# Optimization experiments

Measured on AMD Instinct MI355X. Metric: run time of the kernel, lower is better.

The kernel has to match this reference:

```python
import jax, jax.numpy as jnp
import numpy as np

H_PARAM = 3.0   # filtering strength h
TWS = 5         # template window size
SWS = 11        # search window size


def _shift_stack(x, window_size):
    # [N,C,H,W] -> [N,C,H,W,window_size**2] of circularly shifted copies.
    # Shift order matches the torch module: outer loop x_shift, inner y_shift,
    # roll shifts=(y_shift, x_shift) on dims (H, W).
    r = window_size // 2
    return jnp.stack(
        [jnp.roll(x, (ys, xs), axis=(2, 3))
         for xs in range(-r, r + 1) for ys in range(-r, r + 1)],
        axis=-1,
    )


def _box_filter(x, window_size):
    # Circular box-sum over H,W dims. The torch double roll loop is separable,
    # so do it as two 1-D roll sums (10 rolls instead of 25 for tws=5).
    r = window_size // 2
    s = x
    acc = x
    for k in range(1, r + 1):
        acc = acc + jnp.roll(s, k, axis=3) + jnp.roll(s, -k, axis=3)
    s2 = acc
    for k in range(1, r + 1):
        acc = acc + jnp.roll(s2, k, axis=2) + jnp.roll(s2, -k, axis=2)
    return acc


def setup_inputs() -> dict:
    key = jax.random.key(0)
    x = jax.random.uniform(key, (2, 3, 512, 512), dtype=jnp.float32)
    return {"x": x}


def reference(x):
    # luminance (RGB input: C == 3)
    xc = jnp.clip(x, 0.0, 1.0)
    y = 0.299 * xc[:, :1] + 0.587 * xc[:, 1:2] + 0.114 * xc[:, 2:3]  # [N,1,H,W]

    x_stack = _shift_stack(x, SWS)  # [N,3,H,W,sws^2]
    y_stack = _shift_stack(y, SWS)  # [N,1,H,W,sws^2]

    d2 = _box_filter((y[..., None] - y_stack) ** 2, TWS)  # [N,1,H,W,sws^2]
    distances = jnp.sqrt(d2)
    weights = jnp.exp(-distances / H_PARAM)                # [N,1,H,W,sws^2]

    denoised = (weights * x_stack).sum(axis=-1) / weights.sum(axis=-1)
    return jnp.clip(denoised, 0.0, 1.0)
```

## Files before the change

kernel.cpp:

```cpp
#include <hip/hip_runtime.h>
#include <math.h>


#define H_IMG 512
#define W_IMG 512
#define MASK  511
#define HWSZ  (H_IMG * W_IMG)
#define TILE  32
#define HALO  7
#define XD    46
#define YSTR  48
#define HSTR  44

__global__ __launch_bounds__(256, 2)
void nlm_kernel(const float* __restrict__ x, float* __restrict__ out) {
    __shared__ float4 ldsX[XD * XD];
    __shared__ float  ldsY[XD * YSTR];
    __shared__ float  ldsH[XD * HSTR];

    const int n  = blockIdx.z;
    const int ti = blockIdx.y * TILE;
    const int tj = blockIdx.x * TILE;
    const int tx = threadIdx.x;
    const int ty = threadIdx.y;
    const int tid = ty * 32 + tx;

    const float* xb = x + (size_t)n * 3 * HWSZ;

    for (int e = tid; e < XD * XD; e += 256) {
        int r = e / XD, c = e - r * XD;
        int gi = (ti + r - HALO) & MASK;
        int gj = (tj + c - HALO) & MASK;
        size_t o = (size_t)gi * W_IMG + gj;
        ldsX[e] = make_float4(xb[o], xb[o + HWSZ], xb[o + 2 * HWSZ], 0.f);
    }
    __syncthreads();

    for (int e = tid; e < XD * XD; e += 256) {
        float4 v = ldsX[e];
        float r = fminf(fmaxf(v.x, 0.f), 1.f);
        float g = fminf(fmaxf(v.y, 0.f), 1.f);
        float b = fminf(fmaxf(v.z, 0.f), 1.f);
        int rr = e / XD, cc = e - rr * XD;
        ldsY[rr * YSTR + cc] = 0.299f * r + 0.587f * g + 0.114f * b;
    }
    __syncthreads();

    for (int e = tid; e < XD * 42; e += 256) {
        int r = e / 42, c = e - r * 42;
        const float* yr = &ldsY[r * YSTR + c];
        float a0 = yr[0], a1 = yr[1], a2 = yr[2], a3 = yr[3], a4 = yr[4];
        ldsH[r * HSTR + c] = a0*a0 + a1*a1 + a2*a2 + a3*a3 + a4*a4;
    }
    __syncthreads();

    const int jl = tx + HALO;
    const int il = ty * 4 + HALO;

    float cy[8][5];
    float hc[8];
    #pragma unroll
    for (int t = 0; t < 8; ++t) {
        #pragma unroll
        for (int c = 0; c < 5; ++c)
            cy[t][c] = ldsY[(il - 2 + t) * YSTR + (jl - 2 + c)];
        hc[t] = ldsH[(il - 2 + t) * HSTR + (jl - 2)];
    }

    float den[4]  = {0.f, 0.f, 0.f, 0.f};
    float num0[4] = {0.f, 0.f, 0.f, 0.f};
    float num1[4] = {0.f, 0.f, 0.f, 0.f};
    float num2[4] = {0.f, 0.f, 0.f, 0.f};

    #pragma unroll 1
    for (int xs = -5; xs <= 5; ++xs) {
        const int jc  = jl - xs - 2;
        const int xjc = jl - xs;

        float  sw[8][5];
        float  Hs[8];
        float4 xw[4];

        #pragma unroll
        for (int t = 0; t < 8; ++t) {
            #pragma unroll
            for (int c = 0; c < 5; ++c)
                sw[t][c] = ldsY[(il - 7 + t) * YSTR + jc + c];
            Hs[t] = ldsH[(il - 7 + t) * HSTR + jc];
        }
        #pragma unroll
        for (int t = 0; t < 4; ++t)
            xw[t] = ldsX[(il - 5 + t) * XD + xjc];

        #pragma unroll
        for (int k = 0; k <= 10; ++k) {
            float nsw[5], nHs;
            float4 nxw;
            if (k < 10) {
                const int nr = il + k + 1;
                #pragma unroll
                for (int c = 0; c < 5; ++c) nsw[c] = ldsY[nr * YSTR + jc + c];
                nHs = ldsH[nr * HSTR + jc];
                nxw = ldsX[(il + k - 1) * XD + xjc];
            }

            float h[8];
            #pragma unroll
            for (int t = 0; t < 8; ++t) {
                const int m = (t + k) & 7;
                float s = 0.f;
                #pragma unroll
                for (int c = 0; c < 5; ++c)
                    s = fmaf(cy[t][c], sw[m][c], s);
                h[t] = fmaf(-2.f, s, hc[t] + Hs[m]);
            }

            float d2 = h[0] + h[1] + h[2] + h[3] + h[4];
            #pragma unroll
            for (int o = 0; o < 4; ++o) {
                if (o > 0) d2 += h[o + 4] - h[o - 1];
                float d2c = fmaxf(d2, 0.f);
                float w = __expf(__builtin_amdgcn_sqrtf(d2c) * (-1.0f / 3.0f));
                float4 xv = xw[(k + o) & 3];
                num0[o] = fmaf(w, xv.x, num0[o]);
                num1[o] = fmaf(w, xv.y, num1[o]);
                num2[o] = fmaf(w, xv.z, num2[o]);
                den[o] += w;
            }

            if (k < 10) {
                #pragma unroll
                for (int c = 0; c < 5; ++c) sw[k & 7][c] = nsw[c];
                Hs[k & 7] = nHs;
                xw[k & 3] = nxw;
            }
        }
    }

    float* ob = out + (size_t)n * 3 * HWSZ;
    #pragma unroll
    for (int o = 0; o < 4; ++o) {
        int gi = ti + ty * 4 + o;
        int gj = tj + tx;
        size_t off = (size_t)gi * W_IMG + gj;
        float inv = __builtin_amdgcn_rcpf(den[o]);
        float v0 = fminf(fmaxf(num0[o] * inv, 0.f), 1.f);
        float v1 = fminf(fmaxf(num1[o] * inv, 0.f), 1.f);
        float v2 = fminf(fmaxf(num2[o] * inv, 0.f), 1.f);
        ob[off]            = v0;
        ob[off + HWSZ]     = v1;
        ob[off + 2 * HWSZ] = v2;
    }
}

extern "C" void kernel_launch(void* const* d_in, const int* in_sizes, int n_in,
                              void* d_out, int out_size, void* d_ws, size_t ws_size,
                              hipStream_t stream) {
    const float* x = (const float*)d_in[0];
    float* out = (float*)d_out;
    dim3 grid(W_IMG / TILE, H_IMG / TILE, 2);
    dim3 block(32, 8);
    nlm_kernel<<<grid, block, 0, stream>>>(x, out);
}
```

Measured before the change: 114.4 us.

## Use packed fp16 dot products for patch distances and raise occupancy

Stores luminance as packed half2 pairs in shared memory and computes the patch cross-correlation with fdot2, which cuts the FMA count per shift roughly in half. The template-window sums are restructured into running sliding sums for both the center and shifted squared norms. It also switches to a native exp2 with a folded constant and raises launch bounds to 4 blocks per CU. The fp16 rounding of luminance, combined with the norm-expansion form of the distance, adds cancellation error (it is handled with fabs), and the larger LDS footprint may keep the higher occupancy target from being reached.

```diff
diff --git a/kernel.cpp b/kernel.cpp
--- a/kernel.cpp
+++ b/kernel.cpp
@@ -12,11 +12,30 @@
 #define YSTR  48
 #define HSTR  44
 
-__global__ __launch_bounds__(256, 2)
+typedef _Float16 h2 __attribute__((ext_vector_type(2)));
+
+__device__ __forceinline__ float fdot2(h2 a, h2 b, float c) {
+#if __has_builtin(__builtin_amdgcn_fdot2)
+    return __builtin_amdgcn_fdot2(a, b, c, false);
+#else
+    return c + (float)a.x * (float)b.x + (float)a.y * (float)b.y;
+#endif
+}
+
+__device__ __forceinline__ float fast_exp2(float x) {
+#if __has_builtin(__builtin_amdgcn_exp2f)
+    return __builtin_amdgcn_exp2f(x);
+#else
+    return __expf(x * 0.6931471805599453f);
+#endif
+}
+
+__global__ __launch_bounds__(256, 4)
 void nlm_kernel(const float* __restrict__ x, float* __restrict__ out) {
-    __shared__ float4 ldsX[XD * XD];
-    __shared__ float  ldsY[XD * YSTR];
-    __shared__ float  ldsH[XD * HSTR];
+    __shared__ float4   ldsX[XD * XD];
+    __shared__ float    ldsYf[XD * YSTR];
+    __shared__ unsigned ldsY2[XD * YSTR];
+    __shared__ float    ldsH[XD * HSTR];
 
     const int n  = blockIdx.z;
     const int ti = blockIdx.y * TILE;
@@ -36,35 +55,59 @@
     }
     __syncthreads();
 
+    for (int e = tid; e < XD * 47; e += 256) {
+        int r = e / 47, c = e - r * 47;
+        int cs = (c == 46) ? 45 : c;
+        float4 v = ldsX[r * XD + cs];
+        float rr = fminf(fmaxf(v.x, 0.f), 1.f);
+        float gg = fminf(fmaxf(v.y, 0.f), 1.f);
+        float bb = fminf(fmaxf(v.z, 0.f), 1.f);
+        ldsYf[r * YSTR + c] = 0.299f * rr + 0.587f * gg + 0.114f * bb;
+    }
+    __syncthreads();
+
     for (int e = tid; e < XD * XD; e += 256) {
-        float4 v = ldsX[e];
-        float r = fminf(fmaxf(v.x, 0.f), 1.f);
-        float g = fminf(fmaxf(v.y, 0.f), 1.f);
-        float b = fminf(fmaxf(v.z, 0.f), 1.f);
-        int rr = e / XD, cc = e - rr * XD;
-        ldsY[rr * YSTR + cc] = 0.299f * r + 0.587f * g + 0.114f * b;
+        int r = e / XD, c = e - r * XD;
+        h2 p;
+        p.x = (_Float16)ldsYf[r * YSTR + c];
+        p.y = (_Float16)ldsYf[r * YSTR + c + 1];
+        ldsY2[r * YSTR + c] = __builtin_bit_cast(unsigned, p);
     }
     __syncthreads();
 
     for (int e = tid; e < XD * 42; e += 256) {
         int r = e / 42, c = e - r * 42;
-        const float* yr = &ldsY[r * YSTR + c];
-        float a0 = yr[0], a1 = yr[1], a2 = yr[2], a3 = yr[3], a4 = yr[4];
-        ldsH[r * HSTR + c] = a0*a0 + a1*a1 + a2*a2 + a3*a3 + a4*a4;
+        h2 a  = __builtin_bit_cast(h2, ldsY2[r * YSTR + c]);
+        h2 b  = __builtin_bit_cast(h2, ldsY2[r * YSTR + c + 2]);
+        h2 cc = __builtin_bit_cast(h2, ldsY2[r * YSTR + c + 4]);
+        float x0 = (float)a.x, x1 = (float)a.y;
+        float x2 = (float)b.x, x3 = (float)b.y;
+        float x4 = (float)cc.x;
+        ldsH[r * HSTR + c] = x0*x0 + x1*x1 + x2*x2 + x3*x3 + x4*x4;
     }
     __syncthreads();
 
     const int jl = tx + HALO;
     const int il = ty * 4 + HALO;
 
-    float cy[8][5];
-    float hc[8];
-    #pragma unroll
-    for (int t = 0; t < 8; ++t) {
-        #pragma unroll
-        for (int c = 0; c < 5; ++c)
-            cy[t][c] = ldsY[(il - 2 + t) * YSTR + (jl - 2 + c)];
-        hc[t] = ldsH[(il - 2 + t) * HSTR + (jl - 2)];
+    h2 cyP[8][3];
+    float Vc[4];
+    {
+        float hcv[8];
+        #pragma unroll
+        for (int t = 0; t < 8; ++t) {
+            int base = (il - 2 + t) * YSTR + (jl - 2);
+            cyP[t][0] = __builtin_bit_cast(h2, ldsY2[base]);
+            cyP[t][1] = __builtin_bit_cast(h2, ldsY2[base + 2]);
+            h2 z = __builtin_bit_cast(h2, ldsY2[base + 4]);
+            z.y = (_Float16)0.f;
+            cyP[t][2] = z;
+            hcv[t] = ldsH[(il - 2 + t) * HSTR + (jl - 2)];
+        }
+        Vc[0] = ((hcv[0] + hcv[1]) + (hcv[2] + hcv[3])) + hcv[4];
+        Vc[1] = Vc[0] - hcv[0] + hcv[5];
+        Vc[2] = Vc[1] - hcv[1] + hcv[6];
+        Vc[3] = Vc[2] - hcv[2] + hcv[7];
     }
 
     float den[4]  = {0.f, 0.f, 0.f, 0.f};
@@ -72,55 +115,76 @@
     float num1[4] = {0.f, 0.f, 0.f, 0.f};
     float num2[4] = {0.f, 0.f, 0.f, 0.f};
 
+    const float KEXP = -0.48089834696298783f;
+
     #pragma unroll 1
     for (int xs = -5; xs <= 5; ++xs) {
         const int jc  = jl - xs - 2;
         const int xjc = jl - xs;
 
-        float  sw[8][5];
+        h2     swP[8][3];
         float  Hs[8];
         float4 xw[4];
 
         #pragma unroll
         for (int t = 0; t < 8; ++t) {
-            #pragma unroll
-            for (int c = 0; c < 5; ++c)
-                sw[t][c] = ldsY[(il - 7 + t) * YSTR + jc + c];
+            int base = (il - 7 + t) * YSTR + jc;
+            swP[t][0] = __builtin_bit_cast(h2, ldsY2[base]);
+            swP[t][1] = __builtin_bit_cast(h2, ldsY2[base + 2]);
+            swP[t][2] = __builtin_bit_cast(h2, ldsY2[base + 4]);
             Hs[t] = ldsH[(il - 7 + t) * HSTR + jc];
         }
         #pragma unroll
         for (int t = 0; t < 4; ++t)
             xw[t] = ldsX[(il - 5 + t) * XD + xjc];
 
+        float W0p = 0.f, HsOld = 0.f;
+
         #pragma unroll
         for (int k = 0; k <= 10; ++k) {
-            float nsw[5], nHs;
-            float4 nxw;
+            h2 nsw0, nsw1, nsw2; float nHs; float4 nxw;
             if (k < 10) {
                 const int nr = il + k + 1;
-                #pragma unroll
-                for (int c = 0; c < 5; ++c) nsw[c] = ldsY[nr * YSTR + jc + c];
-                nHs = ldsH[nr * HSTR + jc];
-                nxw = ldsX[(il + k - 1) * XD + xjc];
-            }
-
-            float h[8];
+                int base = nr * YSTR + jc;
+                nsw0 = __builtin_bit_cast(h2, ldsY2[base]);
+                nsw1 = __builtin_bit_cast(h2, ldsY2[base + 2]);
+                nsw2 = __builtin_bit_cast(h2, ldsY2[base + 4]);
+                nHs  = ldsH[nr * HSTR + jc];
+                nxw  = ldsX[(il + k - 1) * XD + xjc];
+            }
+
+            float s[8];
             #pragma unroll
             for (int t = 0; t < 8; ++t) {
                 const int m = (t + k) & 7;
-                float s = 0.f;
-                #pragma unroll
-                for (int c = 0; c < 5; ++c)
-                    s = fmaf(cy[t][c], sw[m][c], s);
-                h[t] = fmaf(-2.f, s, hc[t] + Hs[m]);
-            }
-
-            float d2 = h[0] + h[1] + h[2] + h[3] + h[4];
+                s[t] = fdot2(cyP[t][0], swP[m][0],
+                       fdot2(cyP[t][1], swP[m][1],
+                       fdot2(cyP[t][2], swP[m][2], 0.f)));
+            }
+
+            float S0 = ((s[0] + s[1]) + (s[2] + s[3])) + s[4];
+            float S1 = S0 - s[0] + s[5];
+            float S2 = S1 - s[1] + s[6];
+            float S3 = S2 - s[2] + s[7];
+
+            float W0;
+            if (k == 0) W0 = ((Hs[0] + Hs[1]) + (Hs[2] + Hs[3])) + Hs[4];
+            else        W0 = W0p - HsOld + Hs[(k + 4) & 7];
+            float W1 = W0 - Hs[k & 7]       + Hs[(k + 5) & 7];
+            float W2 = W1 - Hs[(k + 1) & 7] + Hs[(k + 6) & 7];
+            float W3 = W2 - Hs[(k + 2) & 7] + Hs[(k + 7) & 7];
+            W0p = W0;
+
+            float d2a[4];
+            d2a[0] = fmaf(-2.f, S0, Vc[0] + W0);
+            d2a[1] = fmaf(-2.f, S1, Vc[1] + W1);
+            d2a[2] = fmaf(-2.f, S2, Vc[2] + W2);
+            d2a[3] = fmaf(-2.f, S3, Vc[3] + W3);
+
             #pragma unroll
             for (int o = 0; o < 4; ++o) {
-                if (o > 0) d2 += h[o + 4] - h[o - 1];
-                float d2c = fmaxf(d2, 0.f);
-                float w = __expf(__builtin_amdgcn_sqrtf(d2c) * (-1.0f / 3.0f));
+                float sd = __builtin_amdgcn_sqrtf(__builtin_fabsf(d2a[o]));
+                float w  = fast_exp2(KEXP * sd);
                 float4 xv = xw[(k + o) & 3];
                 num0[o] = fmaf(w, xv.x, num0[o]);
                 num1[o] = fmaf(w, xv.y, num1[o]);
@@ -129,8 +193,10 @@
             }
 
             if (k < 10) {
-                #pragma unroll
-                for (int c = 0; c < 5; ++c) sw[k & 7][c] = nsw[c];
+                swP[k & 7][0] = nsw0;
+                swP[k & 7][1] = nsw1;
+                swP[k & 7][2] = nsw2;
+                HsOld = Hs[k & 7];
                 Hs[k & 7] = nHs;
                 xw[k & 3] = nxw;
             }
```

Result: faster. 100.8 us (-11.8%).
